# Optimization experiments

Measured on AMD Instinct MI355X. Metric: run time of the kernel, lower is better.

The kernel has to match this reference:

```python
import jax, jax.numpy as jnp
import numpy as np

EPS_BN = 1e-5
EPS_COS = 1e-8
M_BINS = 10


def _bn(x, g, b):
    # eval-mode BatchNorm2d with running_mean=0, running_var=1
    s = g / jnp.sqrt(1.0 + EPS_BN)
    return x * s[None, :, None, None] + b[None, :, None, None]


def _dw(x, w, pad, dil):
    # depthwise conv, x [B,C,H,W], w [C,1,kh,kw]
    return jax.lax.conv_general_dilated(
        x, w, window_strides=(1, 1), padding=pad, rhs_dilation=dil,
        dimension_numbers=('NCHW', 'OIHW', 'NCHW'),
        feature_group_count=x.shape[1])


def setup_inputs() -> dict:
    key = jax.random.key(0)
    ks = jax.random.split(key, 20)
    B, INP, OUP, H, W = 16, 64, 64, 128, 128
    f32 = jnp.float32
    d = {}
    d['x'] = jax.random.normal(ks[0], (B, INP, H, W), f32)
    d['w_conv1'] = jax.random.normal(ks[1], (OUP, INP), f32) * 0.05
    d['pr_w1'] = jax.random.normal(ks[2], (OUP, 1, 1, 5), f32) * 0.2
    d['pr_w2'] = jax.random.normal(ks[3], (OUP, 1, 5, 1), f32) * 0.2
    d['pr_w3'] = jax.random.normal(ks[4], (OUP, 1, 1, 5), f32) * 0.2
    d['pr_w4'] = jax.random.normal(ks[5], (OUP, 1, 5, 1), f32) * 0.2
    d['pr_gamma'] = 1.0 + 0.1 * jax.random.normal(ks[6], (5, OUP), f32)
    d['pr_beta'] = 0.1 * jax.random.normal(ks[7], (5, OUP), f32)
    d['bn1_g'] = 1.0 + 0.1 * jax.random.normal(ks[8], (OUP,), f32)
    d['bn1_b'] = 0.1 * jax.random.normal(ks[9], (OUP,), f32)
    d['bn2_g'] = 1.0 + 0.1 * jax.random.normal(ks[10], (OUP,), f32)
    d['bn2_b'] = 0.1 * jax.random.normal(ks[11], (OUP,), f32)
    d['fc1_w'] = jax.random.normal(ks[12], (OUP, 2), f32) * 0.5
    d['fc1_b'] = 0.1 * jax.random.normal(ks[13], (OUP,), f32)
    d['phi1_w'] = jax.random.normal(ks[14], (OUP, OUP), f32) * 0.1
    d['phi1_b'] = 0.01 * jax.random.normal(ks[15], (OUP,), f32)
    d['phi2_w'] = jax.random.normal(ks[16], (OUP, OUP), f32) * 0.1
    d['phi2_b'] = 0.01 * jax.random.normal(ks[17], (OUP,), f32)
    d['phi3_w'] = jax.random.normal(ks[18], (OUP, OUP), f32) * 0.1
    d['phi3_b'] = 0.01 * jax.random.normal(ks[19], (OUP,), f32)
    d['w_conv2'] = jax.random.normal(jax.random.fold_in(key, 99), (OUP, 1), f32) * 0.1
    return d


def reference(x, w_conv1, pr_w1, pr_w2, pr_w3, pr_w4, pr_gamma, pr_beta,
              bn1_g, bn1_b, bn2_g, bn2_b, fc1_w, fc1_b,
              phi1_w, phi1_b, phi2_w, phi2_b, phi3_w, phi3_b, w_conv2):
    B, C, H, W = x.shape
    M = M_BINS
    OUP = w_conv1.shape[0]
    # conv1 (1x1) + Position_reinforcement branch
    x_c = jnp.einsum('oc,bchw->bohw', w_conv1, x)
    h = _bn(x_c, pr_gamma[0], pr_beta[0])
    h = _dw(h, pr_w1, ((0, 0), (2, 2)), (1, 1))
    h = _bn(h, pr_gamma[1], pr_beta[1])
    h = _dw(h, pr_w2, ((2, 2), (0, 0)), (1, 1))
    h = _bn(h, pr_gamma[2], pr_beta[2])
    h = _dw(h, pr_w3, ((0, 0), (4, 4)), (2, 2))
    h = _bn(h, pr_gamma[3], pr_beta[3])
    h = _dw(h, pr_w4, ((4, 4), (0, 0)), (2, 2))
    x_center = _bn(h, pr_gamma[4], pr_beta[4])
    # cosine similarity of each pixel feature with the global-avg feature
    g = jnp.mean(x, axis=(2, 3), keepdims=True)             # [B,C,1,1]
    num = jnp.sum(g * x, axis=1)                            # [B,H,W]
    gn = jnp.maximum(jnp.sqrt(jnp.sum(g * g, axis=1)), EPS_COS)
    xn = jnp.maximum(jnp.sqrt(jnp.sum(x * x, axis=1)), EPS_COS)
    S = num / (gn * xn)                                     # [B,H,W]
    Sf = S.reshape(B, H * W)
    # torch casts min/max with float() -> detached constants
    mn = jax.lax.stop_gradient(jnp.min(Sf, axis=1))
    mx = jax.lax.stop_gradient(jnp.max(Sf, axis=1))
    t = jnp.arange(M, dtype=x.dtype) / (M - 1)
    levels = mn[:, None] + (mx - mn)[:, None] * t[None, :]  # [B,M]
    diff = jnp.abs(levels[:, None, :] - Sf[:, :, None])     # [B,HW,M] soft bins
    V = jnp.where(diff < 0.5 / M, 1.0 - diff, jnp.zeros((), x.dtype))
    colsum = jnp.sum(V, axis=1)                             # [B,M]
    # torch normalizes by V.sum() while only columns 0..j are filled -> cumsum
    denom = jnp.cumsum(colsum, axis=1)
    Ch = jnp.stack([colsum / denom, levels], axis=-1)       # [B,M,2]
    Cf = Ch.reshape(-1, 2) @ fc1_w.T + fc1_b                # [B*M,OUP]
    Cq = Cf.reshape(B, OUP, M)                              # raw view as in torch
    p1 = jnp.einsum('oc,bcm->bom', phi1_w, Cq) + phi1_b[None, :, None]
    p2 = jnp.einsum('oc,bcm->bom', phi2_w, Cq) + phi2_b[None, :, None]
    X = jax.nn.softmax(jnp.einsum('bcm,bcn->bmn', p1, p2), axis=-1)  # [B,M,M]
    p3 = jnp.einsum('oc,bcm->bom', phi3_w, Cq) + phi3_b[None, :, None]
    Lp = jnp.einsum('bcm,bmn->bcn', p3, X)                  # [B,OUP,M]
    Vr = V.reshape(B, M, H * W)                             # raw view as in torch
    R = jnp.einsum('bcm,bmk->bck', Lp, Vr).reshape(B, OUP, H, W)
    x_tex = _bn(R, bn1_g, bn1_b)
    x_full = _bn(w_conv2[:, 0][None, :, None, None] * S[:, None, :, :], bn2_g, bn2_b)
    att = jax.nn.sigmoid(x_full + x_tex + x_center)
    return x * att
```

## Files before the change

### kernel.cpp

```cpp
#include <hip/hip_runtime.h>
#include <hip/hip_bf16.h>
#include <math.h>

#define NB   16
#define NC   64
#define NH   128
#define NW   128
#define NHW  16384
#define NM   10
#define XCS  16416

__global__ __launch_bounds__(256) void k_gmean(const float* __restrict__ x,
                                               double* __restrict__ g) {
    int bc = blockIdx.x;
    const float* xp = x + (size_t)bc * NHW;
    double s = 0.0;
    for (int i = threadIdx.x; i < NHW / 4; i += 256) {
        float4 v = ((const float4*)xp)[i];
        s += (double)v.x + (double)v.y + (double)v.z + (double)v.w;
    }
    for (int off = 32; off; off >>= 1) s += __shfl_down(s, off);
    __shared__ double red[4];
    int wid = threadIdx.x >> 6, lane = threadIdx.x & 63;
    if (lane == 0) red[wid] = s;
    __syncthreads();
    if (threadIdx.x == 0)
        g[bc] = (red[0] + red[1] + red[2] + red[3]) * (1.0 / (double)NHW);
}

__global__ __launch_bounds__(256) void k_misc(const float* __restrict__ W,
                                              const double* __restrict__ g,
                                              float* __restrict__ Wt,
                                              double* __restrict__ gn) {
    if (blockIdx.x == 0) {
        for (int e = threadIdx.x; e < 64 * 64; e += 256) {
            int c = e >> 6, o = e & 63;
            Wt[c * 64 + o] = W[o * 64 + c];
        }
    } else if (threadIdx.x == 0) {
        int b = blockIdx.x - 1;
        const double* gb = g + b * NC;
        double gsq = 0.0;
        for (int c = 0; c < NC; ++c) gsq += gb[c] * gb[c];
        gn[b] = fmax(sqrt(gsq), 1e-8);
    }
}

__global__ __launch_bounds__(256, 4) void k_conv1_S(
        const float* __restrict__ x, const float* __restrict__ Wt,
        const double* __restrict__ g, const double* __restrict__ gn,
        float* __restrict__ xc, double* __restrict__ S) {
    int P = blockIdx.x * 256 + threadIdx.x;
    int b = P >> 14, k = P & (NHW - 1);
    const float* xb = x + (size_t)b * NC * NHW + k;

    float xv[NC];
#pragma unroll
    for (int cc = 0; cc < NC; ++cc) {
        int c = ((cc & 1) << 5) | ((cc & 2) << 3) | ((cc & 4) << 1)
              | ((cc & 8) >> 1) | ((cc & 16) >> 3) | ((cc & 32) >> 5);
        xv[c] = xb[(size_t)c * NHW];
    }

    {
        const double* gb = g + b * NC;
        double num = 0.0, sq = 0.0;
#pragma unroll
        for (int c = 0; c < NC; ++c) {
            double v = (double)xv[c];
            num += gb[c] * v;
            sq  += v * v;
        }
        double xn = fmax(sqrt(sq), 1e-8);
        S[P] = num / (gn[b] * xn);
    }

    float* xcb = xc + (size_t)b * NC * XCS + k;
#pragma unroll
    for (int pp = 0; pp < 8; ++pp) {
        int p = ((pp & 1) << 2) | (pp & 2) | ((pp & 4) >> 2);
        int o0 = p * 8;
        float acc[8];
#pragma unroll
        for (int j = 0; j < 8; ++j) acc[j] = 0.f;
#pragma unroll
        for (int c = 0; c < NC; ++c) {
            const float* wr = Wt + c * 64 + o0;
#pragma unroll
            for (int j = 0; j < 8; ++j)
                acc[j] = fmaf(wr[j], xv[c], acc[j]);
        }
#pragma unroll
        for (int j = 0; j < 8; ++j)
            xcb[(size_t)(o0 + j) * XCS] = acc[j];
    }
}

__global__ __launch_bounds__(256) void k_minmax(const double* __restrict__ S,
                                                double* __restrict__ pmn,
                                                double* __restrict__ pmx) {
    int blk = blockIdx.x, b = blk >> 2, part = blk & 3;
    const double* Sb = S + (size_t)b * NHW + part * 4096;
    int tid = threadIdx.x;
    double mn = 1e300, mx = -1e300;
    for (int i = tid; i < 4096; i += 256) {
        double v = Sb[i];
        mn = fmin(mn, v); mx = fmax(mx, v);
    }
    for (int off = 32; off; off >>= 1) {
        mn = fmin(mn, __shfl_down(mn, off));
        mx = fmax(mx, __shfl_down(mx, off));
    }
    __shared__ double rmn[4], rmx[4];
    int wid = tid >> 6, lane = tid & 63;
    if (lane == 0) { rmn[wid] = mn; rmx[wid] = mx; }
    __syncthreads();
    if (tid == 0) {
        pmn[blk] = fmin(fmin(rmn[0], rmn[1]), fmin(rmn[2], rmn[3]));
        pmx[blk] = fmax(fmax(rmx[0], rmx[1]), fmax(rmx[2], rmx[3]));
    }
}

__global__ __launch_bounds__(256) void k_hist(const double* __restrict__ S,
                                              const double* __restrict__ pmn,
                                              const double* __restrict__ pmx,
                                              double* __restrict__ pbins) {
    int blk = blockIdx.x, b = blk >> 2, part = blk & 3;
    double a = fmin(fmin(pmn[4*b], pmn[4*b+1]), fmin(pmn[4*b+2], pmn[4*b+3]));
    double z = fmax(fmax(pmx[4*b], pmx[4*b+1]), fmax(pmx[4*b+2], pmx[4*b+3]));
    double lv[NM];
#pragma unroll
    for (int m = 0; m < NM; ++m) lv[m] = a + (z - a) * ((double)m / 9.0);

    const double* Sb = S + (size_t)b * NHW + part * 4096;
    int tid = threadIdx.x;
    double bins[NM];
#pragma unroll
    for (int m = 0; m < NM; ++m) bins[m] = 0.0;
    for (int i = tid; i < 4096; i += 256) {
        double v = Sb[i];
#pragma unroll
        for (int m = 0; m < NM; ++m) {
            double d = fabs(lv[m] - v);
            if (d < 0.05) bins[m] += 1.0 - d;
        }
    }
#pragma unroll
    for (int m = 0; m < NM; ++m)
        for (int off = 32; off; off >>= 1) bins[m] += __shfl_down(bins[m], off);
    __shared__ double wb[4][NM];
    int wid = tid >> 6, lane = tid & 63;
    if (lane == 0) {
#pragma unroll
        for (int m = 0; m < NM; ++m) wb[wid][m] = bins[m];
    }
    __syncthreads();
    if (tid == 0) {
#pragma unroll
        for (int m = 0; m < NM; ++m)
            pbins[blk * NM + m] = wb[0][m] + wb[1][m] + wb[2][m] + wb[3][m];
    }
}

__global__ __launch_bounds__(256) void k_chain(
        const double* __restrict__ pmn, const double* __restrict__ pmx,
        const double* __restrict__ pbins,
        const float* __restrict__ fc1w, const float* __restrict__ fc1b,
        const float* __restrict__ ph1w, const float* __restrict__ ph1b,
        const float* __restrict__ ph2w, const float* __restrict__ ph2b,
        const float* __restrict__ ph3w, const float* __restrict__ ph3b,
        double* __restrict__ levelsOut, float* __restrict__ LpOut) {
    int b = blockIdx.x, tid = threadIdx.x;
    __shared__ double levS[NM];
    __shared__ float ratio[NM];
    if (tid == 0) {
        double a = fmin(fmin(pmn[4*b], pmn[4*b+1]), fmin(pmn[4*b+2], pmn[4*b+3]));
        double z = fmax(fmax(pmx[4*b], pmx[4*b+1]), fmax(pmx[4*b+2], pmx[4*b+3]));
        for (int m = 0; m < NM; ++m) levS[m] = a + (z - a) * ((double)m / 9.0);
        double den = 0.0;
        for (int m = 0; m < NM; ++m) {
            double cs = ((pbins[(4*b)*NM+m] + pbins[(4*b+1)*NM+m])
                        + pbins[(4*b+2)*NM+m]) + pbins[(4*b+3)*NM+m];
            den += cs;
            ratio[m] = (float)(cs / den);
        }
    }
    __syncthreads();

    __shared__ float CfL[640];
    for (int idx = tid; idx < 640; idx += 256) {
        int rm = idx >> 6, o = idx & 63;
        CfL[idx] = ratio[rm] * fc1w[o*2+0] + (float)levS[rm] * fc1w[o*2+1] + fc1b[o];
    }
    __syncthreads();

    __shared__ float P1[640], P2[640], P3[640];
    for (int idx = tid; idx < 640; idx += 256) {
        int o = idx / 10, m = idx - o * 10;
        float a1 = ph1b[o], a2 = ph2b[o], a3 = ph3b[o];
        for (int c2 = 0; c2 < NC; ++c2) {
            float cq = CfL[c2*10 + m];
            a1 = fmaf(ph1w[o*NC + c2], cq, a1);
            a2 = fmaf(ph2w[o*NC + c2], cq, a2);
            a3 = fmaf(ph3w[o*NC + c2], cq, a3);
        }
        P1[idx] = a1; P2[idx] = a2; P3[idx] = a3;
    }
    __syncthreads();

    __shared__ float XL[100];
    if (tid < 100) {
        int m = tid / 10, n = tid - (tid/10)*10;
        float acc = 0.f;
        for (int c2 = 0; c2 < NC; ++c2)
            acc = fmaf(P1[c2*10 + m], P2[c2*10 + n], acc);
        XL[tid] = acc;
    }
    __syncthreads();
    if (tid < NM) {
        float mxr = XL[tid*10];
        for (int n = 1; n < NM; ++n) mxr = fmaxf(mxr, XL[tid*10 + n]);
        float e[NM], sum = 0.f;
        for (int n = 0; n < NM; ++n) { e[n] = expf(XL[tid*10+n] - mxr); sum += e[n]; }
        for (int n = 0; n < NM; ++n) XL[tid*10+n] = e[n] / sum;
    }
    __syncthreads();

    for (int idx = tid; idx < 640; idx += 256) {
        int c2 = idx / 10, n = idx - (idx/10)*10;
        float acc = 0.f;
#pragma unroll
        for (int m = 0; m < NM; ++m) acc = fmaf(P3[c2*10 + m], XL[m*10 + n], acc);
        LpOut[b*640 + idx] = acc;
    }
    if (tid < NM) levelsOut[b*NM + tid] = levS[tid];
}

__global__ __launch_bounds__(256) void k_vgath(
        const double* __restrict__ S, const double* __restrict__ levels,
        float* __restrict__ vg, float* __restrict__ Sf) {
    int P = blockIdx.x * 256 + threadIdx.x;
    int b = P >> 14, k = P & (NHW - 1);
    __shared__ double levL[NM];
    if (threadIdx.x < NM) levL[threadIdx.x] = levels[b*NM + threadIdx.x];
    __syncthreads();
    const double* Sb = S + (size_t)b * NHW;
    float* vgb = vg + (size_t)b * NM * NHW;
#pragma unroll
    for (int i = 0; i < NM; ++i) {
        int j = i * NHW + k;
        int p = j / 10;
        int m = j - p * 10;
        double d = fabs(levL[m] - Sb[p]);
        vgb[i * NHW + k] = (d < 0.05) ? (float)(1.0 - d) : 0.f;
    }
    Sf[P] = (float)Sb[k];
}

__global__ __launch_bounds__(256) void k_dwfinal(
        const float* __restrict__ xc, const float* __restrict__ x,
        const float* __restrict__ vg, const float* __restrict__ Sf,
        const float* __restrict__ Lp,
        const float* __restrict__ pw1, const float* __restrict__ pw2,
        const float* __restrict__ pw3, const float* __restrict__ pw4,
        const float* __restrict__ gamma, const float* __restrict__ beta,
        const float* __restrict__ bn1g, const float* __restrict__ bn1b,
        const float* __restrict__ bn2g, const float* __restrict__ bn2b,
        const float* __restrict__ wconv2, float* __restrict__ out) {
    int tile = blockIdx.x, c = blockIdx.y, b = blockIdx.z;
    int R0 = (tile >> 1) * 32, C0 = (tile & 1) * 64;
    const float inv = 0.9999950000374997f;
    float s0 = gamma[0*NC+c]*inv, b0 = beta[0*NC+c];
    float s1 = gamma[1*NC+c]*inv, b1 = beta[1*NC+c];
    float s2 = gamma[2*NC+c]*inv, b2 = beta[2*NC+c];
    float s3 = gamma[3*NC+c]*inv, b3 = beta[3*NC+c];
    float s4 = gamma[4*NC+c]*inv, b4 = beta[4*NC+c];
    float w1[5], w2[5], w3[5], w4[5];
#pragma unroll
    for (int q = 0; q < 5; ++q) {
        w1[q] = pw1[c*5+q]; w2[q] = pw2[c*5+q];
        w3[q] = pw3[c*5+q]; w4[q] = pw4[c*5+q];
    }
    float Ac = wconv2[c] * (bn2g[c] * inv);
    float Bc = bn2b[c] + bn1b[c];
    float S1 = bn1g[c] * inv;

    __shared__ __align__(16) float A[44*76];
    __shared__ __align__(16) float Bf[44*72];
    __shared__ float LpL[NM];
    const float* src = xc + (size_t)(b*NC + c) * XCS;
    int tid = threadIdx.x;

    if (tid < NM) LpL[tid] = Lp[b*640 + c*10 + tid];

    for (int t = tid; t < 44*19; t += 256) {
        int r = t / 19, g2 = t - r*19;
        int gy = R0 - 6 + r, gx0 = C0 - 6 + 4*g2;
        float4 v = make_float4(0.f, 0.f, 0.f, 0.f);
        bool rowOK = (unsigned)gy < NH;
        if (rowOK) {
            const float* rowp = src + gy*NW;
            if ((unsigned)gx0 <= (unsigned)(NW-4)) {
                v = *(const float4*)(rowp + gx0);
            } else {
                float* pv = (float*)&v;
#pragma unroll
                for (int u = 0; u < 4; ++u) {
                    int gx = gx0 + u;
                    if ((unsigned)gx < NW) pv[u] = rowp[gx];
                }
            }
        }
        float4 w;
        w.x = (rowOK && (unsigned)(gx0+0) < NW) ? fmaf(v.x, s0, b0) : 0.f;
        w.y = (rowOK && (unsigned)(gx0+1) < NW) ? fmaf(v.y, s0, b0) : 0.f;
        w.z = (rowOK && (unsigned)(gx0+2) < NW) ? fmaf(v.z, s0, b0) : 0.f;
        w.w = (rowOK && (unsigned)(gx0+3) < NW) ? fmaf(v.w, s0, b0) : 0.f;
        *(float4*)&A[r*76 + 4*g2] = w;
    }
    __syncthreads();

    for (int t = tid; t < 44*18; t += 256) {
        int r = t / 18, g2 = t - r*18;
        float xw[8];
        *(float4*)&xw[0] = *(float4*)&A[r*76 + 4*g2];
        *(float4*)&xw[4] = *(float4*)&A[r*76 + 4*g2 + 4];
        int gy = R0 - 6 + r;
        bool rowOK = (unsigned)gy < NH;
        float o[4];
#pragma unroll
        for (int u = 0; u < 4; ++u) {
            float acc = 0.f;
#pragma unroll
            for (int q = 0; q < 5; ++q) acc = fmaf(w1[q], xw[u+q], acc);
            int gx = C0 - 4 + 4*g2 + u;
            o[u] = (rowOK && (unsigned)gx < NW) ? fmaf(acc, s1, b1) : 0.f;
        }
        *(float4*)&Bf[r*72 + 4*g2] = *(float4*)o;
    }
    __syncthreads();

    for (int t = tid; t < 40*18; t += 256) {
        int r = t / 18, g2 = t - r*18;
        float ys[5][4];
#pragma unroll
        for (int p = 0; p < 5; ++p)
            *(float4*)&ys[p][0] = *(float4*)&Bf[(r+p)*72 + 4*g2];
        int gy = R0 - 4 + r;
        bool rowOK = (unsigned)gy < NH;
        float o[4];
#pragma unroll
        for (int u = 0; u < 4; ++u) {
            float acc = 0.f;
#pragma unroll
            for (int p = 0; p < 5; ++p) acc = fmaf(w2[p], ys[p][u], acc);
            int gx = C0 - 4 + 4*g2 + u;
            o[u] = (rowOK && (unsigned)gx < NW) ? fmaf(acc, s2, b2) : 0.f;
        }
        *(float4*)&A[r*72 + 4*g2] = *(float4*)o;
    }
    __syncthreads();

    for (int t = tid; t < 40*16; t += 256) {
        int r = t >> 4, g2 = t & 15;
        float xw[12];
        *(float4*)&xw[0] = *(float4*)&A[r*72 + 4*g2];
        *(float4*)&xw[4] = *(float4*)&A[r*72 + 4*g2 + 4];
        *(float4*)&xw[8] = *(float4*)&A[r*72 + 4*g2 + 8];
        int gy = R0 - 4 + r;
        bool rowOK = (unsigned)gy < NH;
        float o[4];
#pragma unroll
        for (int u = 0; u < 4; ++u) {
            float acc = 0.f;
#pragma unroll
            for (int q = 0; q < 5; ++q) acc = fmaf(w3[q], xw[u+2*q], acc);
            o[u] = rowOK ? fmaf(acc, s3, b3) : 0.f;
        }
        *(float4*)&Bf[r*64 + 4*g2] = *(float4*)o;
    }
    __syncthreads();

    const float* vgb = vg + (size_t)b * NM * NHW;
    const float* Sfb = Sf + (size_t)b * NHW;
    for (int t = tid; t < 32*16; t += 256) {
        int r = t >> 4, g2 = t & 15;
        float ys[5][4];
#pragma unroll
        for (int p = 0; p < 5; ++p)
            *(float4*)&ys[p][0] = *(float4*)&Bf[(r+2*p)*64 + 4*g2];
        int kbase = (R0 + r) * NW + C0 + 4*g2;
        size_t xbase = (size_t)(b*NC + c) * NHW + kbase;
        float4 xv = *(const float4*)&x[xbase];
        float4 skv = *(const float4*)&Sfb[kbase];
        const float* xvp = (const float*)&xv;
        const float* skp = (const float*)&skv;
        float vr[NM][4];
#pragma unroll
        for (int i = 0; i < NM; ++i)
            *(float4*)&vr[i][0] = *(const float4*)&vgb[i * NHW + kbase];
        float res[4];
#pragma unroll
        for (int u = 0; u < 4; ++u) {
            float acc = 0.f;
#pragma unroll
            for (int p = 0; p < 5; ++p) acc = fmaf(w4[p], ys[p][u], acc);
            float xcen = fmaf(acc, s4, b4);
            float R = 0.f;
#pragma unroll
            for (int i = 0; i < NM; ++i) R = fmaf(LpL[i], vr[i][u], R);
            float pre = fmaf(Ac, skp[u], Bc) + S1 * R + xcen;
            float att = 1.0f / (1.0f + expf(-pre));
            res[u] = xvp[u] * att;
        }
        *(float4*)&out[xbase] = *(float4*)res;
    }
}

extern "C" void kernel_launch(void* const* d_in, const int* in_sizes, int n_in,
                              void* d_out, int out_size, void* d_ws, size_t ws_size,
                              hipStream_t stream) {
    (void)in_sizes; (void)n_in; (void)out_size; (void)ws_size;
    const float* x      = (const float*)d_in[0];
    const float* wconv1 = (const float*)d_in[1];
    const float* pw1    = (const float*)d_in[2];
    const float* pw2    = (const float*)d_in[3];
    const float* pw3    = (const float*)d_in[4];
    const float* pw4    = (const float*)d_in[5];
    const float* pgam   = (const float*)d_in[6];
    const float* pbet   = (const float*)d_in[7];
    const float* bn1g   = (const float*)d_in[8];
    const float* bn1b   = (const float*)d_in[9];
    const float* bn2g   = (const float*)d_in[10];
    const float* bn2b   = (const float*)d_in[11];
    const float* fc1w   = (const float*)d_in[12];
    const float* fc1b   = (const float*)d_in[13];
    const float* ph1w   = (const float*)d_in[14];
    const float* ph1b   = (const float*)d_in[15];
    const float* ph2w   = (const float*)d_in[16];
    const float* ph2b   = (const float*)d_in[17];
    const float* ph3w   = (const float*)d_in[18];
    const float* ph3b   = (const float*)d_in[19];
    const float* wconv2 = (const float*)d_in[20];
    float* out = (float*)d_out;

    float*  ws    = (float*)d_ws;
    float*  xc    = ws;
    double* Sd    = (double*)(ws + 1024 * XCS);
    double* g     = Sd + NB * NHW;
    double* lev   = g + NB * NC;
    double* gn    = lev + NB * NM;
    double* pmn   = gn + NB;
    double* pmx   = pmn + 64;
    double* pbins = pmx + 64;
    float*  Lp    = (float*)(pbins + 640);
    float*  vg    = Lp + NB * 640;
    float*  Sf    = vg + NB * NM * NHW;
    float*  Wt    = Sf + NB * NHW;

    k_gmean<<<NB * NC, 256, 0, stream>>>(x, g);
    k_misc<<<17, 256, 0, stream>>>(wconv1, g, Wt, gn);
    k_conv1_S<<<NB * NHW / 256, 256, 0, stream>>>(x, Wt, g, gn, xc, Sd);
    k_minmax<<<NB * 4, 256, 0, stream>>>(Sd, pmn, pmx);
    k_hist<<<NB * 4, 256, 0, stream>>>(Sd, pmn, pmx, pbins);
    k_chain<<<NB, 256, 0, stream>>>(pmn, pmx, pbins, fc1w, fc1b,
                                    ph1w, ph1b, ph2w, ph2b, ph3w, ph3b,
                                    lev, Lp);
    k_vgath<<<NB * NHW / 256, 256, 0, stream>>>(Sd, lev, vg, Sf);
    k_dwfinal<<<dim3(8, NC, NB), 256, 0, stream>>>(
        xc, x, vg, Sf, Lp, pw1, pw2, pw3, pw4, pgam, pbet,
        bn1g, bn1b, bn2g, bn2b, wconv2, out);
}
```

Baseline: 158.0 us.

## Fuse min/max reduction into conv1/S kernel and drop separate minmax pass

Computes per-block min/max of the cosine-similarity map inside the conv1/S kernel, removing the k_minmax launch and its re-read of S. Hist and chain kernels now reduce 64 per-block partials per batch instead of 4. The load order permutation is dropped, the output-channel tiling changes from 8 to 16, and the sigmoid uses fast exp and a hardware reciprocal. The larger accumulator tile may raise register pressure, and the fast math slightly changes precision.

```diff
diff --git a/kernel.cpp b/kernel.cpp
--- a/kernel.cpp
+++ b/kernel.cpp
@@ -49,19 +49,18 @@
 __global__ __launch_bounds__(256, 4) void k_conv1_S(
         const float* __restrict__ x, const float* __restrict__ Wt,
         const double* __restrict__ g, const double* __restrict__ gn,
-        float* __restrict__ xc, double* __restrict__ S) {
-    int P = blockIdx.x * 256 + threadIdx.x;
+        float* __restrict__ xc, double* __restrict__ S,
+        double* __restrict__ pmn, double* __restrict__ pmx) {
+    int bid = blockIdx.x;
+    int P = bid * 256 + threadIdx.x;
     int b = P >> 14, k = P & (NHW - 1);
     const float* xb = x + (size_t)b * NC * NHW + k;
 
     float xv[NC];
 #pragma unroll
-    for (int cc = 0; cc < NC; ++cc) {
-        int c = ((cc & 1) << 5) | ((cc & 2) << 3) | ((cc & 4) << 1)
-              | ((cc & 8) >> 1) | ((cc & 16) >> 3) | ((cc & 32) >> 5);
-        xv[c] = xb[(size_t)c * NHW];
-    }
-
+    for (int c = 0; c < NC; ++c) xv[c] = xb[(size_t)c * NHW];
+
+    double Sv;
     {
         const double* gb = g + b * NC;
         double num = 0.0, sq = 0.0;
@@ -72,52 +71,42 @@
             sq  += v * v;
         }
         double xn = fmax(sqrt(sq), 1e-8);
-        S[P] = num / (gn[b] * xn);
+        Sv = num / (gn[b] * xn);
+        S[P] = Sv;
+    }
+
+    {
+        double mn = Sv, mx = Sv;
+        for (int off = 32; off; off >>= 1) {
+            mn = fmin(mn, __shfl_down(mn, off));
+            mx = fmax(mx, __shfl_down(mx, off));
+        }
+        __shared__ double rmn[4], rmx[4];
+        int wid = threadIdx.x >> 6, lane = threadIdx.x & 63;
+        if (lane == 0) { rmn[wid] = mn; rmx[wid] = mx; }
+        __syncthreads();
+        if (threadIdx.x == 0) {
+            pmn[bid] = fmin(fmin(rmn[0], rmn[1]), fmin(rmn[2], rmn[3]));
+            pmx[bid] = fmax(fmax(rmx[0], rmx[1]), fmax(rmx[2], rmx[3]));
+        }
     }
 
     float* xcb = xc + (size_t)b * NC * XCS + k;
-#pragma unroll
-    for (int pp = 0; pp < 8; ++pp) {
-        int p = ((pp & 1) << 2) | (pp & 2) | ((pp & 4) >> 2);
-        int o0 = p * 8;
-        float acc[8];
-#pragma unroll
-        for (int j = 0; j < 8; ++j) acc[j] = 0.f;
+    for (int p = 0; p < 4; ++p) {
+        int o0 = p * 16;
+        float acc[16];
+#pragma unroll
+        for (int j = 0; j < 16; ++j) acc[j] = 0.f;
 #pragma unroll
         for (int c = 0; c < NC; ++c) {
             const float* wr = Wt + c * 64 + o0;
 #pragma unroll
-            for (int j = 0; j < 8; ++j)
+            for (int j = 0; j < 16; ++j)
                 acc[j] = fmaf(wr[j], xv[c], acc[j]);
         }
 #pragma unroll
-        for (int j = 0; j < 8; ++j)
+        for (int j = 0; j < 16; ++j)
             xcb[(size_t)(o0 + j) * XCS] = acc[j];
-    }
-}
-
-__global__ __launch_bounds__(256) void k_minmax(const double* __restrict__ S,
-                                                double* __restrict__ pmn,
-                                                double* __restrict__ pmx) {
-    int blk = blockIdx.x, b = blk >> 2, part = blk & 3;
-    const double* Sb = S + (size_t)b * NHW + part * 4096;
-    int tid = threadIdx.x;
-    double mn = 1e300, mx = -1e300;
-    for (int i = tid; i < 4096; i += 256) {
-        double v = Sb[i];
-        mn = fmin(mn, v); mx = fmax(mx, v);
-    }
-    for (int off = 32; off; off >>= 1) {
-        mn = fmin(mn, __shfl_down(mn, off));
-        mx = fmax(mx, __shfl_down(mx, off));
-    }
-    __shared__ double rmn[4], rmx[4];
-    int wid = tid >> 6, lane = tid & 63;
-    if (lane == 0) { rmn[wid] = mn; rmx[wid] = mx; }
-    __syncthreads();
-    if (tid == 0) {
-        pmn[blk] = fmin(fmin(rmn[0], rmn[1]), fmin(rmn[2], rmn[3]));
-        pmx[blk] = fmax(fmax(rmx[0], rmx[1]), fmax(rmx[2], rmx[3]));
     }
 }
 
@@ -126,14 +115,23 @@
                                               const double* __restrict__ pmx,
                                               double* __restrict__ pbins) {
     int blk = blockIdx.x, b = blk >> 2, part = blk & 3;
-    double a = fmin(fmin(pmn[4*b], pmn[4*b+1]), fmin(pmn[4*b+2], pmn[4*b+3]));
-    double z = fmax(fmax(pmx[4*b], pmx[4*b+1]), fmax(pmx[4*b+2], pmx[4*b+3]));
+    int tid = threadIdx.x;
+    __shared__ double sa, sz;
+    if (tid < 64) {
+        double mn = pmn[(b << 6) + tid], mx = pmx[(b << 6) + tid];
+        for (int off = 32; off; off >>= 1) {
+            mn = fmin(mn, __shfl_down(mn, off));
+            mx = fmax(mx, __shfl_down(mx, off));
+        }
+        if (tid == 0) { sa = mn; sz = mx; }
+    }
+    __syncthreads();
+    double a = sa, z = sz;
     double lv[NM];
 #pragma unroll
     for (int m = 0; m < NM; ++m) lv[m] = a + (z - a) * ((double)m / 9.0);
 
     const double* Sb = S + (size_t)b * NHW + part * 4096;
-    int tid = threadIdx.x;
     double bins[NM];
 #pragma unroll
     for (int m = 0; m < NM; ++m) bins[m] = 0.0;
@@ -171,11 +169,20 @@
         const float* __restrict__ ph3w, const float* __restrict__ ph3b,
         double* __restrict__ levelsOut, float* __restrict__ LpOut) {
     int b = blockIdx.x, tid = threadIdx.x;
+    __shared__ double sa, sz;
+    if (tid < 64) {
+        double mn = pmn[(b << 6) + tid], mx = pmx[(b << 6) + tid];
+        for (int off = 32; off; off >>= 1) {
+            mn = fmin(mn, __shfl_down(mn, off));
+            mx = fmax(mx, __shfl_down(mx, off));
+        }
+        if (tid == 0) { sa = mn; sz = mx; }
+    }
+    __syncthreads();
     __shared__ double levS[NM];
     __shared__ float ratio[NM];
     if (tid == 0) {
-        double a = fmin(fmin(pmn[4*b], pmn[4*b+1]), fmin(pmn[4*b+2], pmn[4*b+3]));
-        double z = fmax(fmax(pmx[4*b], pmx[4*b+1]), fmax(pmx[4*b+2], pmx[4*b+3]));
+        double a = sa, z = sz;
         for (int m = 0; m < NM; ++m) levS[m] = a + (z - a) * ((double)m / 9.0);
         double den = 0.0;
         for (int m = 0; m < NM; ++m) {
@@ -410,7 +417,8 @@
 #pragma unroll
             for (int i = 0; i < NM; ++i) R = fmaf(LpL[i], vr[i][u], R);
             float pre = fmaf(Ac, skp[u], Bc) + S1 * R + xcen;
-            float att = 1.0f / (1.0f + expf(-pre));
+            float e = __expf(-pre);
+            float att = __builtin_amdgcn_rcpf(1.0f + e);
             res[u] = xvp[u] * att;
         }
         *(float4*)&out[xbase] = *(float4*)res;
@@ -451,8 +459,8 @@
     double* lev   = g + NB * NC;
     double* gn    = lev + NB * NM;
     double* pmn   = gn + NB;
-    double* pmx   = pmn + 64;
-    double* pbins = pmx + 64;
+    double* pmx   = pmn + 1024;
+    double* pbins = pmx + 1024;
     float*  Lp    = (float*)(pbins + 640);
     float*  vg    = Lp + NB * 640;
     float*  Sf    = vg + NB * NM * NHW;
@@ -460,8 +468,8 @@
 
     k_gmean<<<NB * NC, 256, 0, stream>>>(x, g);
     k_misc<<<17, 256, 0, stream>>>(wconv1, g, Wt, gn);
-    k_conv1_S<<<NB * NHW / 256, 256, 0, stream>>>(x, Wt, g, gn, xc, Sd);
-    k_minmax<<<NB * 4, 256, 0, stream>>>(Sd, pmn, pmx);
+    k_conv1_S<<<NB * NHW / 256, 256, 0, stream>>>(x, Wt, g, gn, xc, Sd,
+                                                  pmn, pmx);
     k_hist<<<NB * 4, 256, 0, stream>>>(Sd, pmn, pmx, pbins);
     k_chain<<<NB, 256, 0, stream>>>(pmn, pmx, pbins, fc1w, fc1b,
                                     ph1w, ph1b, ph2w, ph2b, ph3w, ph3b,
```

Measured after the change: 163.2 us. +3.3%, slower.
